# Kernel tuning notes

Hardware: AMD Instinct MI355X
Metric: run time of the kernel (lower is better)

Reference implementation:

```python
import jax, jax.numpy as jnp
import numpy as np

D_MODEL = 1024
N_HEADS = 16
HEAD_DIM = D_MODEL // N_HEADS


def setup_inputs() -> dict:
    key = jax.random.key(0)
    ks = jax.random.split(key, 9)
    B, L = 2, 2048
    s = 1.0 / np.sqrt(D_MODEL)
    return {
        "x": jax.random.normal(ks[0], (B, L, D_MODEL), dtype=jnp.float32),
        "q_w": jax.random.normal(ks[1], (D_MODEL, D_MODEL), dtype=jnp.float32) * s,
        "q_b": jnp.zeros((D_MODEL,), dtype=jnp.float32),
        "k_w": jax.random.normal(ks[2], (D_MODEL, D_MODEL), dtype=jnp.float32) * s,
        "k_b": jnp.zeros((D_MODEL,), dtype=jnp.float32),
        "v_w": jax.random.normal(ks[3], (D_MODEL, D_MODEL), dtype=jnp.float32) * s,
        "v_b": jnp.zeros((D_MODEL,), dtype=jnp.float32),
        "o_w": jax.random.normal(ks[4], (D_MODEL, D_MODEL), dtype=jnp.float32) * s,
        "o_b": jnp.zeros((D_MODEL,), dtype=jnp.float32),
    }


def _rope_tables(L, dtype):
    # inv_freq: [head_dim//2]
    inv_freq = 1.0 / (10000.0 ** (jnp.arange(0, HEAD_DIM, 2, dtype=dtype) / HEAD_DIM))
    t = jnp.arange(L, dtype=dtype)
    freqs = t[:, None] * inv_freq[None, :]          # [L, hd/2]
    emb = jnp.concatenate([freqs, freqs], axis=-1)  # [L, hd]
    return jnp.cos(emb), jnp.sin(emb)


def _rotate_half(x):
    x1, x2 = x[..., : HEAD_DIM // 2], x[..., HEAD_DIM // 2 :]
    return jnp.concatenate([-x2, x1], axis=-1)


def reference(x, q_w, q_b, k_w, k_b, v_w, v_b, o_w, o_b):
    B, L, D = x.shape
    H, hd = N_HEADS, HEAD_DIM
    # Linear (torch: x @ W.T + b), then split heads -> [B, H, L, hd]
    def proj(w, b):
        y = jnp.einsum("bld,ed->ble", x, w) + b
        return y.reshape(B, L, H, hd).transpose(0, 2, 1, 3)

    q, k, v = proj(q_w, q_b), proj(k_w, k_b), proj(v_w, v_b)

    cos, sin = _rope_tables(L, x.dtype)  # [L, hd] each, broadcast over B,H
    q = q * cos + _rotate_half(q) * sin
    k = k * cos + _rotate_half(k) * sin

    scores = jnp.einsum("bhqd,bhkd->bhqk", q, k) / jnp.sqrt(jnp.asarray(hd, x.dtype))
    attn = jax.nn.softmax(scores, axis=-1)
    out = jnp.einsum("bhqk,bhkd->bhqd", attn, v)
    out = out.transpose(0, 2, 1, 3).reshape(B, L, D)
    return jnp.einsum("bld,ed->ble", out, o_w) + o_b
```

## Files before the change

kernel.cpp:

```cpp
#include <hip/hip_runtime.h>
#include <math.h>

#define SEQ   2048
#define NH    16
#define HD    64
#define DM    1024
#define BATCH 2
#define MROWS (BATCH*SEQ)

typedef __attribute__((ext_vector_type(8))) short short8;
typedef __attribute__((ext_vector_type(4))) float f32x4;
typedef unsigned short ushort;

__device__ __forceinline__ ushort f2bf(float x){
  unsigned int u = __float_as_uint(x);
  unsigned int r = (u + 0x7fffu + ((u>>16)&1u)) >> 16;
  return (ushort)r;
}
__device__ __forceinline__ void gload16(const ushort* g, ushort* l){
  __builtin_amdgcn_global_load_lds(
      (const __attribute__((address_space(1))) unsigned int*)(g),
      (__attribute__((address_space(3))) unsigned int*)(l), 16, 0, 0);
}

__global__ void rope_tables_kernel(float* __restrict__ cosT, float* __restrict__ sinT){
  int idx = blockIdx.x*blockDim.x + threadIdx.x;
  if (idx >= SEQ*32) return;
  int i = idx & 31, l = idx >> 5;
  float e = (float)(2*i) / 64.0f;
  float inv = 1.0f / powf(10000.0f, e);
  float ang = (float)l * inv;
  cosT[idx] = cosf(ang);
  sinT[idx] = sinf(ang);
}

__global__ void cast_all_kernel(
    const float* __restrict__ X,
    const float* __restrict__ wq, const float* __restrict__ wk,
    const float* __restrict__ wv, const float* __restrict__ wo,
    ushort* __restrict__ Xh,
    ushort* __restrict__ hq, ushort* __restrict__ hk,
    ushort* __restrict__ hv, ushort* __restrict__ ho)
{
  int idx = blockIdx.x*blockDim.x + threadIdx.x;
  const float* src; ushort* dh; int off;
  const int NX = (MROWS*DM) >> 2;
  if (idx < NX){ src = X; dh = Xh; off = idx; }
  else {
    int t = idx - NX;
    int sel = t >> 18;
    off = t & 262143;
    src = sel==0 ? wq : sel==1 ? wk : sel==2 ? wv : wo;
    dh  = sel==0 ? hq : sel==1 ? hk : sel==2 ? hv : ho;
  }
  float4 v = ((const float4*)src)[off];
  uint2 hp;
  hp.x = (unsigned)f2bf(v.x) | ((unsigned)f2bf(v.y)<<16);
  hp.y = (unsigned)f2bf(v.z) | ((unsigned)f2bf(v.w)<<16);
  ((uint2*)dh)[off] = hp;
}

__global__ __launch_bounds__(256) void gemm_qkv_mfma(
    const ushort* __restrict__ Xh,
    const ushort* __restrict__ Whq, const ushort* __restrict__ Whk, const ushort* __restrict__ Whv,
    const float* __restrict__ bq, const float* __restrict__ bk, const float* __restrict__ bv,
    const float* __restrict__ cosT, const float* __restrict__ sinT,
    ushort* __restrict__ Qb, ushort* __restrict__ Kb, ushort* __restrict__ Vb)
{
  __shared__ __align__(16) ushort As[128*64];
  __shared__ __align__(16) ushort Bs[128*64];
  const int tid = threadIdx.x, w = tid>>6, lane = tid&63;
  const int c = lane & 15, g = lane >> 4;
  const int wr = w >> 1, wc = w & 1;
  const int m0   = blockIdx.x * 128;
  const int ncat = blockIdx.y * 128;
  const int which = ncat >> 10;
  const int n0    = ncat & 1023;
  const ushort* Bhi = which==0 ? Whq : which==1 ? Whk : Whv;
  const float*  bias= which==0 ? bq  : which==1 ? bk  : bv;

  const int srow = lane >> 3;
  const int scol = ((lane & 7) ^ srow) << 3;

  f32x4 acc[4][4] = {};
  for (int k0 = 0; k0 < DM; k0 += 64){
    __syncthreads();
    #pragma unroll
    for (int i=0;i<4;i++){
      const int rb = w*32 + i*8;
      gload16(Xh  + (size_t)(m0 + rb + srow)*DM + k0 + scol, &As[rb*64]);
      gload16(Bhi + (size_t)(n0 + rb + srow)*DM + k0 + scol, &Bs[rb*64]);
    }
    __syncthreads();
    #pragma unroll
    for (int kc=0;kc<2;kc++){
      short8 a[4], b[4];
      #pragma unroll
      for (int m=0;m<4;m++){
        int row = wr*64 + m*16 + c;
        a[m] = *(const short8*)&As[row*64 + ((((kc<<2)+g) ^ (row&7))<<3)];
      }
      #pragma unroll
      for (int n=0;n<4;n++){
        int row = wc*64 + n*16 + c;
        b[n] = *(const short8*)&Bs[row*64 + ((((kc<<2)+g) ^ (row&7))<<3)];
      }
      #pragma unroll
      for (int m=0;m<4;m++)
        #pragma unroll
        for (int n=0;n<4;n++)
          acc[m][n] = __builtin_amdgcn_mfma_f32_16x16x32_bf16(a[m], b[n], acc[m][n], 0,0,0);
    }
  }

  const int hh = (n0 + wc*64) >> 6;
  ushort* Out = which==0 ? Qb : which==1 ? Kb : Vb;
  #pragma unroll
  for (int m=0;m<4;m++){
    #pragma unroll
    for (int r=0;r<4;r++){
      int mrow = m0 + wr*64 + m*16 + 4*g + r;
      int bb = mrow >> 11, l = mrow & (SEQ-1);
      size_t obase = (((size_t)bb*NH + hh)*SEQ + l)*HD;
      size_t vbase = (((size_t)bb*NH + hh)*HD)*SEQ + l;
      #pragma unroll
      for (int n=0;n<2;n++){
        int d1 = n*16 + c, d2 = d1 + 32;
        float v1 = acc[m][n  ][r] + bias[hh*64 + d1];
        float v2 = acc[m][n+2][r] + bias[hh*64 + d2];
        if (which < 2){
          float co = cosT[l*32 + d1], si = sinT[l*32 + d1];
          float o1 = v1*co - v2*si;
          float o2 = v2*co + v1*si;
          if (which == 0){ o1 *= 0.125f; o2 *= 0.125f; }
          Out[obase + d1] = f2bf(o1);
          Out[obase + d2] = f2bf(o2);
        } else {
          Out[vbase + (size_t)d1*SEQ] = f2bf(v1);
          Out[vbase + (size_t)d2*SEQ] = f2bf(v2);
        }
      }
    }
  }
}

__global__ __launch_bounds__(256) void flash_mfma_kernel(
    const ushort* __restrict__ Qb, const ushort* __restrict__ Kb,
    const ushort* __restrict__ VTg, ushort* __restrict__ AOh)
{
  __shared__ __align__(16) ushort Ks[2][64*64];
  __shared__ __align__(16) ushort Vs[2][64*64];
  __shared__ __align__(16) ushort Pl[4][16*64];

  const int tid  = threadIdx.x;
  const int w    = tid >> 6;
  const int lane = tid & 63;
  const int c    = lane & 15;
  const int g    = lane >> 4;
  const int h = blockIdx.y, b = blockIdx.z;
  const int bh = b*NH + h;
  const int q0 = blockIdx.x*64 + w*16;

  const int srow   = lane >> 3;
  const int sgran8 = ((lane & 7) ^ srow) << 3;
  const int rb0 = w*16, rb1 = w*16 + 8;

  const ushort* Kbase = Kb  + (size_t)bh*SEQ*HD;
  const ushort* Vbase = VTg + (size_t)bh*HD*SEQ;

  const ushort* Qrow = Qb + ((size_t)bh*SEQ + (q0 + c))*HD;
  const short8 qf0 = *(const short8*)(Qrow + 8*g);
  const short8 qf1 = *(const short8*)(Qrow + 32 + 8*g);

  const f32x4 vzero = {0.f,0.f,0.f,0.f};
  f32x4 oacc[4] = {vzero, vzero, vzero, vzero};
  float ssum[4] = {0.f,0.f,0.f,0.f};

  gload16(Kbase + (size_t)(rb0 + srow)*HD + sgran8, &Ks[0][rb0*64]);
  gload16(Kbase + (size_t)(rb1 + srow)*HD + sgran8, &Ks[0][rb1*64]);
  gload16(Vbase + (size_t)(rb0 + srow)*SEQ + sgran8, &Vs[0][rb0*64]);
  gload16(Vbase + (size_t)(rb1 + srow)*SEQ + sgran8, &Vs[0][rb1*64]);
  __syncthreads();

  int buf = 0;
  for (int t0 = 0; t0 < SEQ; t0 += 64){
    if (t0 + 64 < SEQ){
      const int nb = buf ^ 1, t1 = t0 + 64;
      gload16(Kbase + (size_t)(t1 + rb0 + srow)*HD + sgran8, &Ks[nb][rb0*64]);
      gload16(Kbase + (size_t)(t1 + rb1 + srow)*HD + sgran8, &Ks[nb][rb1*64]);
      gload16(Vbase + (size_t)(rb0 + srow)*SEQ + t1 + sgran8, &Vs[nb][rb0*64]);
      gload16(Vbase + (size_t)(rb1 + srow)*SEQ + t1 + sgran8, &Vs[nb][rb1*64]);
    }

    f32x4 s[4];
    __builtin_amdgcn_s_setprio(1);
    #pragma unroll
    for (int n=0;n<4;n++){
      int j = 16*n + c;
      short8 k0 = *(const short8*)&Ks[buf][j*64 + ((g     ^ (j&7))<<3)];
      short8 k1 = *(const short8*)&Ks[buf][j*64 + (((4+g) ^ (j&7))<<3)];
      f32x4 z = vzero;
      z = __builtin_amdgcn_mfma_f32_16x16x32_bf16(qf0, k0, z, 0,0,0);
      z = __builtin_amdgcn_mfma_f32_16x16x32_bf16(qf1, k1, z, 0,0,0);
      s[n] = z;
    }
    __builtin_amdgcn_s_setprio(0);

    #pragma unroll
    for (int n=0;n<4;n++){
      #pragma unroll
      for (int r=0;r<4;r++){
        float p = __expf(s[n][r]);
        ssum[r] += p;
        int q = 4*g + r;
        Pl[w][q*64 + ((16*n+c) ^ ((q&7)<<3))] = f2bf(p);
      }
    }

    short8 pa0 = *(const short8*)&Pl[w][c*64 + (( 8*g   ) ^ ((c&7)<<3))];
    short8 pa1 = *(const short8*)&Pl[w][c*64 + ((32+8*g) ^ ((c&7)<<3))];
    __builtin_amdgcn_s_setprio(1);
    #pragma unroll
    for (int nd=0;nd<4;nd++){
      int d = 16*nd + c;
      short8 v0 = *(const short8*)&Vs[buf][d*64 + ((g     ^ (d&7))<<3)];
      short8 v1 = *(const short8*)&Vs[buf][d*64 + (((4+g) ^ (d&7))<<3)];
      oacc[nd] = __builtin_amdgcn_mfma_f32_16x16x32_bf16(pa0, v0, oacc[nd], 0,0,0);
      oacc[nd] = __builtin_amdgcn_mfma_f32_16x16x32_bf16(pa1, v1, oacc[nd], 0,0,0);
    }
    __builtin_amdgcn_s_setprio(0);

    __syncthreads();
    buf ^= 1;
  }

  #pragma unroll
  for (int r=0;r<4;r++){
    float v = ssum[r];
    v += __shfl_xor(v, 1);
    v += __shfl_xor(v, 2);
    v += __shfl_xor(v, 4);
    v += __shfl_xor(v, 8);
    ssum[r] = 1.0f / v;
  }

  #pragma unroll
  for (int nd=0;nd<4;nd++){
    #pragma unroll
    for (int r=0;r<4;r++){
      int q = q0 + 4*g + r;
      int d = 16*nd + c;
      AOh[((size_t)b*SEQ + q)*DM + h*HD + d] = f2bf(oacc[nd][r] * ssum[r]);
    }
  }
}

__global__ __launch_bounds__(256) void gemm_o_mfma(
    const ushort* __restrict__ AOh, const ushort* __restrict__ Who,
    const float* __restrict__ bo, float* __restrict__ Y)
{
  __shared__ __align__(16) ushort As[128*64];
  __shared__ __align__(16) ushort Bs[128*64];
  const int tid = threadIdx.x, w = tid>>6, lane = tid&63;
  const int c = lane & 15, g = lane >> 4;
  const int wr = w >> 1, wc = w & 1;
  const int m0 = blockIdx.x * 128;
  const int n0 = blockIdx.y * 128;

  const int srow = lane >> 3;
  const int scol = ((lane & 7) ^ srow) << 3;

  f32x4 acc[4][4] = {};
  for (int k0 = 0; k0 < DM; k0 += 64){
    __syncthreads();
    #pragma unroll
    for (int i=0;i<4;i++){
      const int rb = w*32 + i*8;
      gload16(AOh + (size_t)(m0 + rb + srow)*DM + k0 + scol, &As[rb*64]);
      gload16(Who + (size_t)(n0 + rb + srow)*DM + k0 + scol, &Bs[rb*64]);
    }
    __syncthreads();
    #pragma unroll
    for (int kc=0;kc<2;kc++){
      short8 a[4], b[4];
      #pragma unroll
      for (int m=0;m<4;m++){
        int row = wr*64 + m*16 + c;
        a[m] = *(const short8*)&As[row*64 + ((((kc<<2)+g) ^ (row&7))<<3)];
      }
      #pragma unroll
      for (int n=0;n<4;n++){
        int row = wc*64 + n*16 + c;
        b[n] = *(const short8*)&Bs[row*64 + ((((kc<<2)+g) ^ (row&7))<<3)];
      }
      #pragma unroll
      for (int m=0;m<4;m++)
        #pragma unroll
        for (int n=0;n<4;n++)
          acc[m][n] = __builtin_amdgcn_mfma_f32_16x16x32_bf16(a[m], b[n], acc[m][n], 0,0,0);
    }
  }

  #pragma unroll
  for (int m=0;m<4;m++){
    #pragma unroll
    for (int r=0;r<4;r++){
      int mrow = m0 + wr*64 + m*16 + 4*g + r;
      #pragma unroll
      for (int n=0;n<4;n++){
        int ncol = n0 + wc*64 + n*16 + c;
        Y[(size_t)mrow*DM + ncol] = acc[m][n][r] + bo[ncol];
      }
    }
  }
}

extern "C" void kernel_launch(void* const* d_in, const int* in_sizes, int n_in,
                              void* d_out, int out_size, void* d_ws, size_t ws_size,
                              hipStream_t stream)
{
  const float* x  = (const float*)d_in[0];
  const float* qw = (const float*)d_in[1];
  const float* qb = (const float*)d_in[2];
  const float* kw = (const float*)d_in[3];
  const float* kb = (const float*)d_in[4];
  const float* vw = (const float*)d_in[5];
  const float* vb = (const float*)d_in[6];
  const float* ow = (const float*)d_in[7];
  const float* ob = (const float*)d_in[8];
  float* out = (float*)d_out;

  const size_t NE = (size_t)MROWS*DM;
  const size_t WE = (size_t)DM*DM;
  float* cosT = (float*)d_ws;
  float* sinT = cosT + SEQ*32;
  ushort* p = (ushort*)(sinT + SEQ*32);
  ushort* Xh  = p;            p += NE;
  ushort* Whq = p;            p += WE;
  ushort* Whk = p;            p += WE;
  ushort* Whv = p;            p += WE;
  ushort* Who = p;            p += WE;
  ushort* Qb  = p;            p += NE;
  ushort* Kb  = p;            p += NE;
  ushort* Vb  = p;            p += NE;
  ushort* AOh = p;            p += NE;

  hipLaunchKernelGGL(rope_tables_kernel, dim3((SEQ*32+255)/256), dim3(256), 0, stream, cosT, sinT);
  hipLaunchKernelGGL(cast_all_kernel, dim3((NE/4 + WE)/256), dim3(256), 0, stream,
                     x, qw, kw, vw, ow, Xh, Whq, Whk, Whv, Who);
  hipLaunchKernelGGL(gemm_qkv_mfma, dim3(MROWS/128, 3072/128), dim3(256), 0, stream,
                     Xh, Whq, Whk, Whv, qb, kb, vb, cosT, sinT, Qb, Kb, Vb);
  hipLaunchKernelGGL(flash_mfma_kernel, dim3(SEQ/64, NH, BATCH), dim3(256), 0, stream,
                     Qb, Kb, Vb, AOh);
  hipLaunchKernelGGL(gemm_o_mfma, dim3(MROWS/128, DM/128), dim3(256), 0, stream,
                     AOh, Who, ob, out);
}
```

Baseline: 142.1 us.

## Switch flash attention to 32x32 MFMA with register-resident P and MFMA row sums

Rewrites the attention inner loop to use 32x32x16 bf16 MFMA, with each wave owning 32 query rows and each block 128 rows. S is computed transposed (K as A operand), so P can be packed to bf16 and redistributed with v_permlane32_swap instead of a round trip through an LDS staging buffer. Row sums are computed by an extra MFMA against a vector of ones rather than scalar adds and shuffles. This halves the grid and removes the P LDS traffic, at the cost of more registers and fewer blocks for latency hiding.

```diff
diff --git a/kernel.cpp b/kernel.cpp
--- a/kernel.cpp
+++ b/kernel.cpp
@@ -10,7 +10,9 @@
 
 typedef __attribute__((ext_vector_type(8))) short short8;
 typedef __attribute__((ext_vector_type(4))) float f32x4;
+typedef __attribute__((ext_vector_type(16))) float f32x16;
 typedef unsigned short ushort;
+typedef unsigned int uint;
 
 __device__ __forceinline__ ushort f2bf(float x){
   unsigned int u = __float_as_uint(x);
@@ -150,16 +152,15 @@
 {
   __shared__ __align__(16) ushort Ks[2][64*64];
   __shared__ __align__(16) ushort Vs[2][64*64];
-  __shared__ __align__(16) ushort Pl[4][16*64];
 
   const int tid  = threadIdx.x;
   const int w    = tid >> 6;
   const int lane = tid & 63;
-  const int c    = lane & 15;
-  const int g    = lane >> 4;
-  const int h = blockIdx.y, b = blockIdx.z;
-  const int bh = b*NH + h;
-  const int q0 = blockIdx.x*64 + w*16;
+  const int c    = lane & 31;
+  const int h    = lane >> 5;
+  const int hd = blockIdx.y, b = blockIdx.z;
+  const int bh = b*NH + hd;
+  const int q0 = blockIdx.x*128 + w*32;
 
   const int srow   = lane >> 3;
   const int sgran8 = ((lane & 7) ^ srow) << 3;
@@ -168,13 +169,17 @@
   const ushort* Kbase = Kb  + (size_t)bh*SEQ*HD;
   const ushort* Vbase = VTg + (size_t)bh*HD*SEQ;
 
-  const ushort* Qrow = Qb + ((size_t)bh*SEQ + (q0 + c))*HD;
-  const short8 qf0 = *(const short8*)(Qrow + 8*g);
-  const short8 qf1 = *(const short8*)(Qrow + 32 + 8*g);
-
-  const f32x4 vzero = {0.f,0.f,0.f,0.f};
-  f32x4 oacc[4] = {vzero, vzero, vzero, vzero};
-  float ssum[4] = {0.f,0.f,0.f,0.f};
+  const ushort* Qrow = Qb + ((size_t)bh*SEQ + q0 + c)*HD + 8*h;
+  short8 qf[4];
+  #pragma unroll
+  for (int kc=0;kc<4;kc++) qf[kc] = *(const short8*)(Qrow + kc*16);
+
+  short8 ones;
+  #pragma unroll
+  for (int i=0;i<8;i++) ones[i] = (short)0x3F80;
+
+  f32x16 oacc[2] = {};
+  f32x16 sacc = {};
 
   gload16(Kbase + (size_t)(rb0 + srow)*HD + sgran8, &Ks[0][rb0*64]);
   gload16(Kbase + (size_t)(rb1 + srow)*HD + sgran8, &Ks[0][rb1*64]);
@@ -192,65 +197,60 @@
       gload16(Vbase + (size_t)(rb1 + srow)*SEQ + t1 + sgran8, &Vs[nb][rb1*64]);
     }
 
-    f32x4 s[4];
-    __builtin_amdgcn_s_setprio(1);
-    #pragma unroll
-    for (int n=0;n<4;n++){
-      int j = 16*n + c;
-      short8 k0 = *(const short8*)&Ks[buf][j*64 + ((g     ^ (j&7))<<3)];
-      short8 k1 = *(const short8*)&Ks[buf][j*64 + (((4+g) ^ (j&7))<<3)];
-      f32x4 z = vzero;
-      z = __builtin_amdgcn_mfma_f32_16x16x32_bf16(qf0, k0, z, 0,0,0);
-      z = __builtin_amdgcn_mfma_f32_16x16x32_bf16(qf1, k1, z, 0,0,0);
-      s[n] = z;
-    }
-    __builtin_amdgcn_s_setprio(0);
-
-    #pragma unroll
-    for (int n=0;n<4;n++){
-      #pragma unroll
-      for (int r=0;r<4;r++){
-        float p = __expf(s[n][r]);
-        ssum[r] += p;
-        int q = 4*g + r;
-        Pl[w][q*64 + ((16*n+c) ^ ((q&7)<<3))] = f2bf(p);
-      }
-    }
-
-    short8 pa0 = *(const short8*)&Pl[w][c*64 + (( 8*g   ) ^ ((c&7)<<3))];
-    short8 pa1 = *(const short8*)&Pl[w][c*64 + ((32+8*g) ^ ((c&7)<<3))];
-    __builtin_amdgcn_s_setprio(1);
-    #pragma unroll
-    for (int nd=0;nd<4;nd++){
-      int d = 16*nd + c;
-      short8 v0 = *(const short8*)&Vs[buf][d*64 + ((g     ^ (d&7))<<3)];
-      short8 v1 = *(const short8*)&Vs[buf][d*64 + (((4+g) ^ (d&7))<<3)];
-      oacc[nd] = __builtin_amdgcn_mfma_f32_16x16x32_bf16(pa0, v0, oacc[nd], 0,0,0);
-      oacc[nd] = __builtin_amdgcn_mfma_f32_16x16x32_bf16(pa1, v1, oacc[nd], 0,0,0);
-    }
-    __builtin_amdgcn_s_setprio(0);
+    #pragma unroll
+    for (int kb=0; kb<2; kb++){
+      f32x16 s = {};
+      __builtin_amdgcn_s_setprio(1);
+      #pragma unroll
+      for (int kc=0;kc<4;kc++){
+        int row = kb*32 + c;
+        short8 kf = *(const short8*)&Ks[buf][row*64 + (((2*kc + h) ^ (row&7))<<3)];
+        s = __builtin_amdgcn_mfma_f32_32x32x16_bf16(kf, qf[kc], s, 0,0,0);
+      }
+      __builtin_amdgcn_s_setprio(0);
+
+      uint pk[8];
+      #pragma unroll
+      for (int i=0;i<8;i++){
+        float p0 = __expf(s[2*i]);
+        float p1 = __expf(s[2*i+1]);
+        asm("v_cvt_pk_bf16_f32 %0, %1, %2" : "=v"(pk[i]) : "v"(p0), "v"(p1));
+      }
+      asm volatile("v_permlane32_swap_b32 %0, %1" : "+v"(pk[0]), "+v"(pk[2]));
+      asm volatile("v_permlane32_swap_b32 %0, %1" : "+v"(pk[1]), "+v"(pk[3]));
+      asm volatile("v_permlane32_swap_b32 %0, %1" : "+v"(pk[4]), "+v"(pk[6]));
+      asm volatile("v_permlane32_swap_b32 %0, %1" : "+v"(pk[5]), "+v"(pk[7]));
+      short8 pa0, pa1;
+      ((uint*)&pa0)[0]=pk[0]; ((uint*)&pa0)[1]=pk[1]; ((uint*)&pa0)[2]=pk[2]; ((uint*)&pa0)[3]=pk[3];
+      ((uint*)&pa1)[0]=pk[4]; ((uint*)&pa1)[1]=pk[5]; ((uint*)&pa1)[2]=pk[6]; ((uint*)&pa1)[3]=pk[7];
+
+      __builtin_amdgcn_s_setprio(1);
+      #pragma unroll
+      for (int db=0; db<2; db++){
+        int vrow = db*32 + c;
+        short8 v0 = *(const short8*)&Vs[buf][vrow*64 + (((4*kb     + h) ^ (vrow&7))<<3)];
+        short8 v1 = *(const short8*)&Vs[buf][vrow*64 + (((4*kb + 2 + h) ^ (vrow&7))<<3)];
+        oacc[db] = __builtin_amdgcn_mfma_f32_32x32x16_bf16(pa0, v0, oacc[db], 0,0,0);
+        oacc[db] = __builtin_amdgcn_mfma_f32_32x32x16_bf16(pa1, v1, oacc[db], 0,0,0);
+      }
+      sacc = __builtin_amdgcn_mfma_f32_32x32x16_bf16(pa0, ones, sacc, 0,0,0);
+      sacc = __builtin_amdgcn_mfma_f32_32x32x16_bf16(pa1, ones, sacc, 0,0,0);
+      __builtin_amdgcn_s_setprio(0);
+    }
 
     __syncthreads();
     buf ^= 1;
   }
 
-  #pragma unroll
-  for (int r=0;r<4;r++){
-    float v = ssum[r];
-    v += __shfl_xor(v, 1);
-    v += __shfl_xor(v, 2);
-    v += __shfl_xor(v, 4);
-    v += __shfl_xor(v, 8);
-    ssum[r] = 1.0f / v;
-  }
-
-  #pragma unroll
-  for (int nd=0;nd<4;nd++){
-    #pragma unroll
-    for (int r=0;r<4;r++){
-      int q = q0 + 4*g + r;
-      int d = 16*nd + c;
-      AOh[((size_t)b*SEQ + q)*DM + h*HD + d] = f2bf(oacc[nd][r] * ssum[r]);
+  float inv[16];
+  #pragma unroll
+  for (int r=0;r<16;r++) inv[r] = 1.0f / sacc[r];
+  #pragma unroll
+  for (int db=0; db<2; db++){
+    #pragma unroll
+    for (int r=0;r<16;r++){
+      int q = q0 + (r&3) + 8*(r>>2) + 4*h;
+      AOh[((size_t)b*SEQ + q)*DM + hd*HD + db*32 + c] = f2bf(oacc[db][r] * inv[r]);
     }
   }
 }
@@ -350,7 +350,7 @@
                      x, qw, kw, vw, ow, Xh, Whq, Whk, Whv, Who);
   hipLaunchKernelGGL(gemm_qkv_mfma, dim3(MROWS/128, 3072/128), dim3(256), 0, stream,
                      Xh, Whq, Whk, Whv, qb, kb, vb, cosT, sinT, Qb, Kb, Vb);
-  hipLaunchKernelGGL(flash_mfma_kernel, dim3(SEQ/64, NH, BATCH), dim3(256), 0, stream,
+  hipLaunchKernelGGL(flash_mfma_kernel, dim3(SEQ/128, NH, BATCH), dim3(256), 0, stream,
                      Qb, Kb, Vb, AOh);
   hipLaunchKernelGGL(gemm_o_mfma, dim3(MROWS/128, DM/128), dim3(256), 0, stream,
                      AOh, Who, ob, out);
```

Measured after the change: 133.5 us. 6.1% less time.
